# Kernel tuning notes

Hardware: AMD Instinct MI355X
Metric: run time of the kernel (lower is better)

## Reference

```python
import jax, jax.numpy as jnp
import numpy as np

N = 32768      # nodes
E = 524288     # edges (before self-loops)
F_IN = 256     # input feature dim
H = 4          # attention heads
C = 128        # per-head (and output) channels; concat=False -> mean over heads
NEG_SLOPE = 0.2
BN_EPS = 1e-5


def setup_inputs() -> dict:
    key = jax.random.key(0)
    ks = jax.random.split(key, 20)
    s = 0.1
    inp = {
        "x": jax.random.normal(ks[0], (N, F_IN), dtype=jnp.float32),
        "edge_index": jax.random.randint(ks[1], (2, E), 0, N, dtype=jnp.int64),
        # layer 1 (GATConv in=256 -> heads=4, C=128) + BN
        "W1": jax.random.normal(ks[2], (F_IN, H * C), dtype=jnp.float32) * s,
        "as1": jax.random.normal(ks[3], (H, C), dtype=jnp.float32) * s,
        "ad1": jax.random.normal(ks[4], (H, C), dtype=jnp.float32) * s,
        "b1": jnp.zeros((C,), jnp.float32),
        "g1": jnp.ones((C,), jnp.float32),
        "be1": jnp.zeros((C,), jnp.float32),
        # layer 2 (GATConv in=128 -> heads=4, C=128) + BN
        "W2": jax.random.normal(ks[5], (C, H * C), dtype=jnp.float32) * s,
        "as2": jax.random.normal(ks[6], (H, C), dtype=jnp.float32) * s,
        "ad2": jax.random.normal(ks[7], (H, C), dtype=jnp.float32) * s,
        "b2": jnp.zeros((C,), jnp.float32),
        "g2": jnp.ones((C,), jnp.float32),
        "be2": jnp.zeros((C,), jnp.float32),
        # final linear C -> C
        "Wf": jax.random.normal(ks[8], (C, C), dtype=jnp.float32) * s,
        "bf": jnp.zeros((C,), jnp.float32),
    }
    return inp


def _gat_conv(x, src, dst, W, att_src, att_dst, bias):
    # x: [N, Din]; src/dst: [E'] (self-loops already included)
    h = (x @ W).reshape(N, H, C)                     # [N,H,C]
    a_src = jnp.sum(h * att_src, axis=-1)            # [N,H]
    a_dst = jnp.sum(h * att_dst, axis=-1)            # [N,H]
    e = jax.nn.leaky_relu(a_src[src] + a_dst[dst], NEG_SLOPE)  # [E',H]
    # softmax over incoming edges per destination node (segment softmax)
    m = jax.ops.segment_max(e, dst, num_segments=N)  # [N,H]; safe: self-loops
    e = jnp.exp(e - m[dst])
    denom = jax.ops.segment_sum(e, dst, num_segments=N)
    alpha = e / (denom[dst] + 1e-16)                 # [E',H]
    msg = h[src] * alpha[:, :, None]                 # [E',H,C]
    out = jax.ops.segment_sum(msg, dst, num_segments=N)  # [N,H,C]
    return out.mean(axis=1) + bias                   # concat=False -> head mean


def _batch_norm(x, gamma, beta):
    mu = x.mean(axis=0)
    var = x.var(axis=0)  # biased, as torch BN normalization
    return (x - mu) * jax.lax.rsqrt(var + BN_EPS) * gamma + beta


def reference(x, edge_index, W1, as1, ad1, b1, g1, be1,
              W2, as2, ad2, b2, g2, be2, Wf, bf):
    # add self-loops (PyG GATConv default add_self_loops=True)
    loop = jnp.arange(N, dtype=edge_index.dtype)
    src = jnp.concatenate([edge_index[0], loop])
    dst = jnp.concatenate([edge_index[1], loop])

    h = _gat_conv(x, src, dst, W1, as1, ad1, b1)
    h = jax.nn.relu(_batch_norm(h, g1, be1))  # dropout = identity (eval)

    h = _gat_conv(h, src, dst, W2, as2, ad2, b2)
    h = jax.nn.relu(_batch_norm(h, g2, be2))

    return h @ Wf + bf
```

## Files before the change

### kernel.cpp

```cpp
#include <hip/hip_runtime.h>
#include <math.h>

namespace {

constexpr int N    = 32768;
constexpr int E    = 524288;
constexpr int ETOT = E + N;
constexpr int FIN  = 256;
constexpr int H    = 4;
constexpr int C    = 128;
constexpr int HC   = H * C;
constexpr float NEG    = 0.2f;
constexpr float BN_EPS = 1e-5f;

typedef __attribute__((ext_vector_type(8))) short  bf16x8;
typedef __attribute__((ext_vector_type(4))) float  f32x4;

__device__ __forceinline__ float lrelu(float x) { return x >= 0.f ? x : NEG * x; }

__device__ __forceinline__ unsigned short f2b(float f) {
  unsigned u = __float_as_uint(f);
  u = (u + 0x7fffu + ((u >> 16) & 1u)) >> 16;
  return (unsigned short)u;
}
__device__ __forceinline__ unsigned pack2(float a, float b) {
  return (unsigned)f2b(a) | ((unsigned)f2b(b) << 16);
}
__device__ __forceinline__ float blo(unsigned u) { return __uint_as_float(u << 16); }
__device__ __forceinline__ float bhi(unsigned u) { return __uint_as_float(u & 0xffff0000u); }

__device__ __forceinline__ void gll16(const unsigned short* g, unsigned short* l) {
  __builtin_amdgcn_global_load_lds(
      (const __attribute__((address_space(1))) unsigned int*)g,
      (__attribute__((address_space(3))) unsigned int*)l, 16, 0, 0);
}

__global__ void k_cvt4(const float* __restrict__ in, unsigned short* __restrict__ out, int n4) {
  int i = blockIdx.x * blockDim.x + threadIdx.x;
  if (i >= n4) return;
  float4 v = reinterpret_cast<const float4*>(in)[i];
  ushort4 o;
  o.x = f2b(v.x); o.y = f2b(v.y); o.z = f2b(v.z); o.w = f2b(v.w);
  reinterpret_cast<ushort4*>(out)[i] = o;
}

__global__ void k_wcvt(const float* __restrict__ W, unsigned short* __restrict__ Wt,
                       int K, int Nc) {
  int idx = blockIdx.x * blockDim.x + threadIdx.x;
  if (idx >= K * Nc) return;
  int c = idx / K, k = idx - c * K;
  Wt[idx] = f2b(W[(size_t)k * Nc + c]);
}

__global__ void k_wstack(const float* __restrict__ W, unsigned short* __restrict__ Bt,
                         int Din) {
  int idx = blockIdx.x * blockDim.x + threadIdx.x;
  if (idx >= C * 4 * Din) return;
  int c = idx / (4 * Din), r = idx - c * (4 * Din);
  int h = r / Din, k = r - h * Din;
  Bt[idx] = f2b(W[(size_t)k * HC + h * C + c]);
}

__global__ void k_attvec(const float* __restrict__ W, const float* __restrict__ as_,
                         const float* __restrict__ ad_, float* __restrict__ av, int Din) {
  int idx = blockIdx.x * blockDim.x + threadIdx.x;
  if (idx >= 8 * Din) return;
  int j = idx / Din, k = idx - j * Din, h = j & 3;
  const float* a = (j < 4) ? as_ : ad_;
  float s = 0.f;
  for (int c = 0; c < C; ++c) s += W[(size_t)k * HC + h * C + c] * a[h * C + c];
  av[idx] = s;
}

template<int DIN>
__global__ __launch_bounds__(256) void k_attdots(
    const unsigned short* __restrict__ xb, const float* __restrict__ av,
    float* __restrict__ asrc, float* __restrict__ adst)
{
  constexpr int CPL = DIN / 64;
  __shared__ float avs[8 * DIN];
  for (int i = threadIdx.x; i < 8 * DIN; i += 256) avs[i] = av[i];
  __syncthreads();
  int wid = threadIdx.x >> 6, lane = threadIdx.x & 63;
  int n = blockIdx.x * 4 + wid;
  float xv[CPL];
  if constexpr (CPL == 4) {
    uint2 u = *reinterpret_cast<const uint2*>(&xb[(size_t)n * DIN + lane * 4]);
    xv[0] = blo(u.x); xv[1] = bhi(u.x); xv[2] = blo(u.y); xv[3] = bhi(u.y);
  } else {
    unsigned u = *reinterpret_cast<const unsigned*>(&xb[(size_t)n * DIN + lane * 2]);
    xv[0] = blo(u); xv[1] = bhi(u);
  }
  float s[8];
#pragma unroll
  for (int j = 0; j < 8; ++j) {
    float t = 0.f;
#pragma unroll
    for (int q = 0; q < CPL; ++q) t += xv[q] * avs[j * DIN + lane * CPL + q];
    s[j] = t;
  }
#pragma unroll
  for (int off = 1; off < 64; off <<= 1)
#pragma unroll
    for (int j = 0; j < 8; ++j) s[j] += __shfl_xor(s[j], off);
  if (lane == 0) {
    *reinterpret_cast<float4*>(&asrc[n * 4]) = make_float4(s[0], s[1], s[2], s[3]);
    *reinterpret_cast<float4*>(&adst[n * 4]) = make_float4(s[4], s[5], s[6], s[7]);
  }
}

__global__ void k_deg(const int* __restrict__ edst, int* __restrict__ deg) {
  int e = blockIdx.x * blockDim.x + threadIdx.x;
  if (e >= ETOT) return;
  int d = (e < E) ? edst[e] : (e - E);
  atomicAdd(&deg[d], 1);
}

__global__ __launch_bounds__(1024) void k_scan(const int* __restrict__ deg,
                                               int* __restrict__ offs) {
  __shared__ int sums[1024];
  int t = threadIdx.x;
  int base = t * 32;
  int local[32];
  int tot = 0;
#pragma unroll
  for (int i = 0; i < 32; ++i) { local[i] = deg[base + i]; tot += local[i]; }
  sums[t] = tot;
  __syncthreads();
  for (int off = 1; off < 1024; off <<= 1) {
    int v = (t >= off) ? sums[t - off] : 0;
    __syncthreads();
    sums[t] += v;
    __syncthreads();
  }
  int run = (t == 0) ? 0 : sums[t - 1];
#pragma unroll
  for (int i = 0; i < 32; ++i) { offs[base + i] = run; run += local[i]; }
  if (t == 1023) offs[N] = run;
}

__global__ void k_scatter(const int* __restrict__ esrc, const int* __restrict__ edst,
                          const int* __restrict__ offs, int* __restrict__ cursor,
                          int* __restrict__ csrc) {
  int e = blockIdx.x * blockDim.x + threadIdx.x;
  if (e >= ETOT) return;
  int s = (e < E) ? esrc[e] : (e - E);
  int d = (e < E) ? edst[e] : (e - E);
  int pos = offs[d] + atomicAdd(&cursor[d], 1);
  csrc[pos] = s;
}

template<int DIN>
__global__ __launch_bounds__(256) void k_fused_agg(
    const unsigned short* __restrict__ xb, const int* __restrict__ offs,
    const int* __restrict__ csrc, const float* __restrict__ asrc,
    const float* __restrict__ adst, unsigned short* __restrict__ z)
{
  constexpr int CPL = DIN / 64;
  __shared__ float pls[4][64][4];
  __shared__ int   sls[4][64];
  const int wid = threadIdx.x >> 6, lane = threadIdx.x & 63;
  const int n = blockIdx.x * 4 + wid;
  const int beg = offs[n], end = offs[n + 1];
  const float4 bv = *reinterpret_cast<const float4*>(&adst[n * 4]);

  float d0 = 0.f, d1 = 0.f, d2 = 0.f, d3 = 0.f;
  float acc[4][CPL] = {};
  for (int base = beg; base < end; base += 64) {
    int i = base + lane;
    float p0 = 0.f, p1 = 0.f, p2 = 0.f, p3 = 0.f;
    int s = 0;
    if (i < end) {
      s = csrc[i];
      float4 av = *reinterpret_cast<const float4*>(&asrc[s * 4]);
      p0 = __expf(lrelu(av.x + bv.x));
      p1 = __expf(lrelu(av.y + bv.y));
      p2 = __expf(lrelu(av.z + bv.z));
      p3 = __expf(lrelu(av.w + bv.w));
    }
    sls[wid][lane] = s;
    *reinterpret_cast<float4*>(&pls[wid][lane][0]) = make_float4(p0, p1, p2, p3);
    d0 += p0; d1 += p1; d2 += p2; d3 += p3;
    int cnt = end - base; if (cnt > 64) cnt = 64;
#pragma unroll 4
    for (int j = 0; j < cnt; ++j) {
      int sj = sls[wid][j];
      float4 pj = *reinterpret_cast<const float4*>(&pls[wid][j][0]);
      if constexpr (CPL == 4) {
        uint2 u = *reinterpret_cast<const uint2*>(&xb[(size_t)sj * DIN + lane * 4]);
        float c0 = blo(u.x), c1 = bhi(u.x), c2 = blo(u.y), c3 = bhi(u.y);
        acc[0][0] += pj.x * c0; acc[0][1] += pj.x * c1; acc[0][2] += pj.x * c2; acc[0][3] += pj.x * c3;
        acc[1][0] += pj.y * c0; acc[1][1] += pj.y * c1; acc[1][2] += pj.y * c2; acc[1][3] += pj.y * c3;
        acc[2][0] += pj.z * c0; acc[2][1] += pj.z * c1; acc[2][2] += pj.z * c2; acc[2][3] += pj.z * c3;
        acc[3][0] += pj.w * c0; acc[3][1] += pj.w * c1; acc[3][2] += pj.w * c2; acc[3][3] += pj.w * c3;
      } else {
        unsigned u = *reinterpret_cast<const unsigned*>(&xb[(size_t)sj * DIN + lane * 2]);
        float c0 = blo(u), c1 = bhi(u);
        acc[0][0] += pj.x * c0; acc[0][1] += pj.x * c1;
        acc[1][0] += pj.y * c0; acc[1][1] += pj.y * c1;
        acc[2][0] += pj.z * c0; acc[2][1] += pj.z * c1;
        acc[3][0] += pj.w * c0; acc[3][1] += pj.w * c1;
      }
    }
  }
#pragma unroll
  for (int off = 1; off < 64; off <<= 1) {
    d0 += __shfl_xor(d0, off);
    d1 += __shfl_xor(d1, off);
    d2 += __shfl_xor(d2, off);
    d3 += __shfl_xor(d3, off);
  }
  float inv[4];
  inv[0] = 0.25f / (d0 + 1e-16f); inv[1] = 0.25f / (d1 + 1e-16f);
  inv[2] = 0.25f / (d2 + 1e-16f); inv[3] = 0.25f / (d3 + 1e-16f);
  size_t zb = (size_t)n * 4 * DIN;
#pragma unroll
  for (int h = 0; h < 4; ++h) {
    if constexpr (CPL == 4) {
      uint2 o;
      o.x = pack2(acc[h][0] * inv[h], acc[h][1] * inv[h]);
      o.y = pack2(acc[h][2] * inv[h], acc[h][3] * inv[h]);
      *reinterpret_cast<uint2*>(&z[zb + h * DIN + lane * 4]) = o;
    } else {
      *reinterpret_cast<unsigned*>(&z[zb + h * DIN + lane * 2]) =
          pack2(acc[h][0] * inv[h], acc[h][1] * inv[h]);
    }
  }
}

__global__ __launch_bounds__(256) void gemm_bt(
    const unsigned short* __restrict__ A,
    const unsigned short* __restrict__ Bt,
    const float* __restrict__ bias,
    float* __restrict__ O, int K)
{
  __shared__ unsigned short As[64 * 32];
  __shared__ unsigned short Bs[128 * 32];
  const int tid  = threadIdx.x;
  const int wave = tid >> 6, lane = tid & 63;
  const int wr = (wave >> 1) * 32, wc = (wave & 1) * 64;
  const int row0 = blockIdx.x * 64;

  const int fr = lane & 15, kqc = lane >> 4;
  const int sl_r = lane >> 2;
  const int sl_c = lane & 3;

  const int ra  = (wave << 4) + sl_r;
  const int ca  = (sl_c ^ ((ra >> 1) & 3)) * 8;
  const int rb0 = (wave << 5) + sl_r;
  const int cb0 = (sl_c ^ ((rb0 >> 1) & 3)) * 8;
  const int rb1 = rb0 + 16;
  const int cb1 = (sl_c ^ ((rb1 >> 1) & 3)) * 8;

  f32x4 acc[2][4] = {};
  for (int k0 = 0; k0 < K; k0 += 32) {
    gll16(&A [(size_t)(row0 + ra) * K + k0 + ca ], &As[(size_t)(wave << 4) * 32]);
    gll16(&Bt[(size_t)rb0         * K + k0 + cb0], &Bs[(size_t)(wave << 5) * 32]);
    gll16(&Bt[(size_t)rb1         * K + k0 + cb1], &Bs[(size_t)((wave << 5) + 16) * 32]);
    __syncthreads();

    bf16x8 af[2], bfr[4];
#pragma unroll
    for (int m = 0; m < 2; ++m) {
      int r = wr + m * 16 + fr;
      af[m] = *(const bf16x8*)&As[r * 32 + (kqc ^ ((r >> 1) & 3)) * 8];
    }
#pragma unroll
    for (int nn = 0; nn < 4; ++nn) {
      int r = wc + nn * 16 + fr;
      bfr[nn] = *(const bf16x8*)&Bs[r * 32 + (kqc ^ ((r >> 1) & 3)) * 8];
    }
#pragma unroll
    for (int m = 0; m < 2; ++m)
#pragma unroll
      for (int nn = 0; nn < 4; ++nn)
        acc[m][nn] = __builtin_amdgcn_mfma_f32_16x16x32_bf16(af[m], bfr[nn], acc[m][nn], 0, 0, 0);
    __syncthreads();
  }

  const int fq = (lane >> 4) * 4;
#pragma unroll
  for (int m = 0; m < 2; ++m)
#pragma unroll
    for (int nn = 0; nn < 4; ++nn) {
      int col = wc + nn * 16 + fr;
      float bv = bias ? bias[col] : 0.f;
#pragma unroll
      for (int j = 0; j < 4; ++j) {
        int row = row0 + wr + m * 16 + fq + j;
        O[(size_t)row * 128 + col] = acc[m][nn][j] + bv;
      }
    }
}

__global__ __launch_bounds__(128) void k_bn_stats(const float* __restrict__ x,
                                                  float* __restrict__ stats) {
  int c = threadIdx.x;
  int rows = N / gridDim.x;
  int r0 = blockIdx.x * rows;
  float s = 0.f, s2 = 0.f;
  for (int r = r0; r < r0 + rows; ++r) {
    float v = x[(size_t)r * C + c];
    s += v; s2 += v * v;
  }
  atomicAdd(&stats[c], s);
  atomicAdd(&stats[C + c], s2);
}

__global__ void k_bn_apply(const float* __restrict__ stats, const float* __restrict__ g,
                           const float* __restrict__ be, const float* __restrict__ xin,
                           unsigned short* __restrict__ xb) {
  int i = blockIdx.x * blockDim.x + threadIdx.x;
  if (i >= N * C) return;
  int c = i & (C - 1);
  float mu  = stats[c] * (1.f / N);
  float var = stats[C + c] * (1.f / N) - mu * mu;
  float v = (xin[i] - mu) * rsqrtf(var + BN_EPS) * g[c] + be[c];
  xb[i] = f2b(v > 0.f ? v : 0.f);
}

}

extern "C" void kernel_launch(void* const* d_in, const int* in_sizes, int n_in,
                              void* d_out, int out_size, void* d_ws, size_t ws_size,
                              hipStream_t stream) {
  const float* x   = (const float*)d_in[0];
  const int*   ei  = (const int*)d_in[1];
  const float* W1  = (const float*)d_in[2];
  const float* as1 = (const float*)d_in[3];
  const float* ad1 = (const float*)d_in[4];
  const float* g1  = (const float*)d_in[6];
  const float* be1 = (const float*)d_in[7];
  const float* W2  = (const float*)d_in[8];
  const float* as2 = (const float*)d_in[9];
  const float* ad2 = (const float*)d_in[10];
  const float* g2  = (const float*)d_in[12];
  const float* be2 = (const float*)d_in[13];
  const float* Wf  = (const float*)d_in[14];
  const float* bf  = (const float*)d_in[15];
  float* out = (float*)d_out;

  const int* esrc = ei;
  const int* edst = ei + E;

  char* p = (char*)d_ws;
  auto alloc = [&](size_t bytes) {
    char* r = p;
    p += (bytes + 255) & ~size_t(255);
    return r;
  };
  unsigned short* z1   = (unsigned short*)alloc(2ull * N * 4 * FIN);
  unsigned short* xbf  = (unsigned short*)alloc(2ull * N * FIN);
  unsigned short* xmb  = (unsigned short*)alloc(2ull * N * C);
  float*    xm     = (float*)alloc(sizeof(float) * (size_t)N * C);
  unsigned short* Wst1 = (unsigned short*)alloc(2ull * C * 4 * FIN);
  unsigned short* Wst2 = (unsigned short*)alloc(2ull * C * 4 * C);
  unsigned short* Wft  = (unsigned short*)alloc(2ull * C * C);
  float*    av1    = (float*)alloc(sizeof(float) * 8 * FIN);
  float*    av2    = (float*)alloc(sizeof(float) * 8 * C);
  float*    asrc   = (float*)alloc(sizeof(float) * N * 4);
  float*    adst   = (float*)alloc(sizeof(float) * N * 4);
  float*    stats  = (float*)alloc(sizeof(float) * 2 * C);
  int*      deg    = (int*)alloc(sizeof(int) * N);
  int*      offs   = (int*)alloc(sizeof(int) * (N + 16));
  int*      cursor = (int*)alloc(sizeof(int) * N);
  int*      csrc   = (int*)alloc(sizeof(int) * ETOT);
  (void)ws_size; (void)in_sizes; (void)n_in; (void)out_size;

  const int EB = (ETOT + 255) / 256;

  hipMemsetAsync(deg, 0, sizeof(int) * N, stream);
  hipMemsetAsync(cursor, 0, sizeof(int) * N, stream);
  k_deg<<<EB, 256, 0, stream>>>(edst, deg);
  k_scan<<<1, 1024, 0, stream>>>(deg, offs);
  k_scatter<<<EB, 256, 0, stream>>>(esrc, edst, offs, cursor, csrc);

  k_cvt4<<<(N * FIN / 4 + 255) / 256, 256, 0, stream>>>(x, xbf, N * FIN / 4);
  k_wstack<<<(C * 4 * FIN + 255) / 256, 256, 0, stream>>>(W1, Wst1, FIN);
  k_wstack<<<(C * 4 * C + 255) / 256, 256, 0, stream>>>(W2, Wst2, C);
  k_wcvt<<<(C * C + 255) / 256, 256, 0, stream>>>(Wf, Wft, C, C);
  k_attvec<<<(8 * FIN + 255) / 256, 256, 0, stream>>>(W1, as1, ad1, av1, FIN);
  k_attvec<<<(8 * C + 255) / 256, 256, 0, stream>>>(W2, as2, ad2, av2, C);

  k_attdots<FIN><<<N / 4, 256, 0, stream>>>(xbf, av1, asrc, adst);
  k_fused_agg<FIN><<<N / 4, 256, 0, stream>>>(xbf, offs, csrc, asrc, adst, z1);
  gemm_bt<<<N / 64, 256, 0, stream>>>(z1, Wst1, nullptr, xm, 4 * FIN);
  hipMemsetAsync(stats, 0, sizeof(float) * 2 * C, stream);
  k_bn_stats<<<256, C, 0, stream>>>(xm, stats);
  k_bn_apply<<<(N * C) / 256, 256, 0, stream>>>(stats, g1, be1, xm, xmb);

  k_attdots<C><<<N / 4, 256, 0, stream>>>(xmb, av2, asrc, adst);
  k_fused_agg<C><<<N / 4, 256, 0, stream>>>(xmb, offs, csrc, asrc, adst, z1);
  gemm_bt<<<N / 64, 256, 0, stream>>>(z1, Wst2, nullptr, xm, 4 * C);
  hipMemsetAsync(stats, 0, sizeof(float) * 2 * C, stream);
  k_bn_stats<<<256, C, 0, stream>>>(xm, stats);
  k_bn_apply<<<(N * C) / 256, 256, 0, stream>>>(stats, g2, be2, xm, xmb);

  gemm_bt<<<N / 64, 256, 0, stream>>>(xmb, Wft, bf, out, C);
}
```

Baseline: 455.5 us.

## Merge prep kernels, fuse BN-apply into attention dots, split edge softmax into pass

Folds all setup conversions, weight stacking, attention-vector precompute and buffer zeroing into one k_prep launch, replacing several small kernels and memsets. Fuses the layer-1 BN apply and ReLU into the layer-2 attention-dot kernel, which also writes the bf16 activations. Moves the edge exp and denominator work out of the aggregation into a separate k_eexp pass that writes per-edge weights and inverse denominators to a buffer. This cuts launch overhead and shortens the aggregation's critical loop, at the cost of an extra pass that writes and rereads per-edge weights. The aggregation loads csrc and pbuf past the segment end without bounds checks, covered by padded allocations.

```diff
diff --git a/kernel.cpp b/kernel.cpp
--- a/kernel.cpp
+++ b/kernel.cpp
@@ -35,41 +35,89 @@
       (__attribute__((address_space(3))) unsigned int*)l, 16, 0, 0);
 }
 
-__global__ void k_cvt4(const float* __restrict__ in, unsigned short* __restrict__ out, int n4) {
-  int i = blockIdx.x * blockDim.x + threadIdx.x;
-  if (i >= n4) return;
-  float4 v = reinterpret_cast<const float4*>(in)[i];
-  ushort4 o;
-  o.x = f2b(v.x); o.y = f2b(v.y); o.z = f2b(v.z); o.w = f2b(v.w);
-  reinterpret_cast<ushort4*>(out)[i] = o;
-}
-
-__global__ void k_wcvt(const float* __restrict__ W, unsigned short* __restrict__ Wt,
-                       int K, int Nc) {
-  int idx = blockIdx.x * blockDim.x + threadIdx.x;
-  if (idx >= K * Nc) return;
-  int c = idx / K, k = idx - c * K;
-  Wt[idx] = f2b(W[(size_t)k * Nc + c]);
-}
-
-__global__ void k_wstack(const float* __restrict__ W, unsigned short* __restrict__ Bt,
-                         int Din) {
-  int idx = blockIdx.x * blockDim.x + threadIdx.x;
-  if (idx >= C * 4 * Din) return;
-  int c = idx / (4 * Din), r = idx - c * (4 * Din);
-  int h = r / Din, k = r - h * Din;
-  Bt[idx] = f2b(W[(size_t)k * HC + h * C + c]);
-}
-
-__global__ void k_attvec(const float* __restrict__ W, const float* __restrict__ as_,
-                         const float* __restrict__ ad_, float* __restrict__ av, int Din) {
-  int idx = blockIdx.x * blockDim.x + threadIdx.x;
-  if (idx >= 8 * Din) return;
-  int j = idx / Din, k = idx - j * Din, h = j & 3;
-  const float* a = (j < 4) ? as_ : ad_;
-  float s = 0.f;
-  for (int c = 0; c < C; ++c) s += W[(size_t)k * HC + h * C + c] * a[h * C + c];
-  av[idx] = s;
+constexpr int PB_X   = (N * FIN / 4) / 256;
+constexpr int PB_W1  = (C * 4 * FIN) / 256;
+constexpr int PB_W2  = (C * 4 * C) / 256;
+constexpr int PB_WF  = (C * C) / 256;
+constexpr int PB_AV1 = (8 * FIN) / 256;
+constexpr int PB_AV2 = (8 * C) / 256;
+constexpr int PB_Z   = (2 * N + 512) / 256;
+constexpr int PB_TOT = PB_X + PB_W1 + PB_W2 + PB_WF + PB_AV1 + PB_AV2 + PB_Z;
+
+__global__ __launch_bounds__(256) void k_prep(
+    const float* __restrict__ x,
+    const float* __restrict__ W1, const float* __restrict__ W2, const float* __restrict__ Wf,
+    const float* __restrict__ as1, const float* __restrict__ ad1,
+    const float* __restrict__ as2, const float* __restrict__ ad2,
+    unsigned short* __restrict__ xbf, unsigned short* __restrict__ Wst1,
+    unsigned short* __restrict__ Wst2, unsigned short* __restrict__ Wft,
+    float* __restrict__ av1, float* __restrict__ av2,
+    int* __restrict__ deg, int* __restrict__ cursor,
+    float* __restrict__ stats1, float* __restrict__ stats2)
+{
+  int b = blockIdx.x, t = threadIdx.x;
+  if (b < PB_X) {
+    int i = b * 256 + t;
+    float4 v = reinterpret_cast<const float4*>(x)[i];
+    ushort4 o;
+    o.x = f2b(v.x); o.y = f2b(v.y); o.z = f2b(v.z); o.w = f2b(v.w);
+    reinterpret_cast<ushort4*>(xbf)[i] = o;
+    return;
+  }
+  b -= PB_X;
+  if (b < PB_W1) {
+    int idx = b * 256 + t;
+    int c = idx / (4 * FIN), r = idx - c * (4 * FIN);
+    int h = r / FIN, k = r - h * FIN;
+    Wst1[idx] = f2b(W1[(size_t)k * HC + h * C + c]);
+    return;
+  }
+  b -= PB_W1;
+  if (b < PB_W2) {
+    int idx = b * 256 + t;
+    int c = idx / (4 * C), r = idx - c * (4 * C);
+    int h = r / C, k = r - h * C;
+    Wst2[idx] = f2b(W2[(size_t)k * HC + h * C + c]);
+    return;
+  }
+  b -= PB_W2;
+  if (b < PB_WF) {
+    int idx = b * 256 + t;
+    int c = idx / C, k = idx - c * C;
+    Wft[idx] = f2b(Wf[(size_t)k * C + c]);
+    return;
+  }
+  b -= PB_WF;
+  if (b < PB_AV1) {
+    int idx = b * 256 + t;
+    int j = idx / FIN, k = idx - j * FIN, h = j & 3;
+    const float* a = (j < 4) ? as1 : ad1;
+    float s = 0.f;
+    for (int c = 0; c < C; ++c) s += W1[(size_t)k * HC + h * C + c] * a[h * C + c];
+    av1[idx] = s;
+    return;
+  }
+  b -= PB_AV1;
+  if (b < PB_AV2) {
+    int idx = b * 256 + t;
+    int j = idx / C, k = idx - j * C, h = j & 3;
+    const float* a = (j < 4) ? as2 : ad2;
+    float s = 0.f;
+    for (int c = 0; c < C; ++c) s += W2[(size_t)k * HC + h * C + c] * a[h * C + c];
+    av2[idx] = s;
+    return;
+  }
+  b -= PB_AV2;
+  {
+    int i = b * 256 + t;
+    if (i < N) deg[i] = 0;
+    else if (i < 2 * N) cursor[i - N] = 0;
+    else {
+      int i2 = i - 2 * N;
+      if (i2 < 256) stats1[i2] = 0.f;
+      else if (i2 < 512) stats2[i2 - 256] = 0.f;
+    }
+  }
 }
 
 template<int DIN>
@@ -109,6 +157,45 @@
   }
 }
 
+__global__ __launch_bounds__(256) void k_attdots_bn(
+    const float* __restrict__ xm, const float* __restrict__ stats,
+    const float* __restrict__ g, const float* __restrict__ be,
+    const float* __restrict__ av, unsigned short* __restrict__ xmb,
+    float* __restrict__ asrc, float* __restrict__ adst)
+{
+  __shared__ float avs[8 * C];
+  __shared__ float bnsc[C], bnsh[C];
+  int t = threadIdx.x;
+  for (int i = t; i < 8 * C; i += 256) avs[i] = av[i];
+  if (t < C) {
+    float mu  = stats[t] * (1.f / N);
+    float var = stats[C + t] * (1.f / N) - mu * mu;
+    float sc  = rsqrtf(var + BN_EPS) * g[t];
+    bnsc[t] = sc;
+    bnsh[t] = be[t] - mu * sc;
+  }
+  __syncthreads();
+  int wid = t >> 6, lane = t & 63;
+  int n = blockIdx.x * 4 + wid;
+  int c = lane * 2;
+  float2 xv = *reinterpret_cast<const float2*>(&xm[(size_t)n * C + c]);
+  float v0 = fmaxf(xv.x * bnsc[c]     + bnsh[c],     0.f);
+  float v1 = fmaxf(xv.y * bnsc[c + 1] + bnsh[c + 1], 0.f);
+  *reinterpret_cast<unsigned*>(&xmb[(size_t)n * C + c]) = pack2(v0, v1);
+  float s[8];
+#pragma unroll
+  for (int j = 0; j < 8; ++j)
+    s[j] = v0 * avs[j * C + c] + v1 * avs[j * C + c + 1];
+#pragma unroll
+  for (int off = 1; off < 64; off <<= 1)
+#pragma unroll
+    for (int j = 0; j < 8; ++j) s[j] += __shfl_xor(s[j], off);
+  if (lane == 0) {
+    *reinterpret_cast<float4*>(&asrc[n * 4]) = make_float4(s[0], s[1], s[2], s[3]);
+    *reinterpret_cast<float4*>(&adst[n * 4]) = make_float4(s[4], s[5], s[6], s[7]);
+  }
+}
+
 __global__ void k_deg(const int* __restrict__ edst, int* __restrict__ deg) {
   int e = blockIdx.x * blockDim.x + threadIdx.x;
   if (e >= ETOT) return;
@@ -150,11 +237,44 @@
   csrc[pos] = s;
 }
 
+__global__ __launch_bounds__(256) void k_eexp(
+    const int* __restrict__ offs, const int* __restrict__ csrc,
+    const float* __restrict__ asrc, const float* __restrict__ adst,
+    float* __restrict__ pbuf, float* __restrict__ denominv)
+{
+  int gid = blockIdx.x * 256 + threadIdx.x;
+  int n = gid >> 4, l = gid & 15;
+  int beg = offs[n], end = offs[n + 1];
+  const float4 bv = *reinterpret_cast<const float4*>(&adst[n * 4]);
+  float d0 = 0.f, d1 = 0.f, d2 = 0.f, d3 = 0.f;
+  for (int i = beg + l; i < end; i += 16) {
+    int s = csrc[i];
+    float4 av = *reinterpret_cast<const float4*>(&asrc[s * 4]);
+    float p0 = __expf(lrelu(av.x + bv.x));
+    float p1 = __expf(lrelu(av.y + bv.y));
+    float p2 = __expf(lrelu(av.z + bv.z));
+    float p3 = __expf(lrelu(av.w + bv.w));
+    *reinterpret_cast<float4*>(&pbuf[(size_t)i * 4]) = make_float4(p0, p1, p2, p3);
+    d0 += p0; d1 += p1; d2 += p2; d3 += p3;
+  }
+#pragma unroll
+  for (int off = 1; off < 16; off <<= 1) {
+    d0 += __shfl_xor(d0, off);
+    d1 += __shfl_xor(d1, off);
+    d2 += __shfl_xor(d2, off);
+    d3 += __shfl_xor(d3, off);
+  }
+  if (l == 0)
+    *reinterpret_cast<float4*>(&denominv[n * 4]) =
+        make_float4(0.25f / (d0 + 1e-16f), 0.25f / (d1 + 1e-16f),
+                    0.25f / (d2 + 1e-16f), 0.25f / (d3 + 1e-16f));
+}
+
 template<int DIN>
 __global__ __launch_bounds__(256) void k_fused_agg(
     const unsigned short* __restrict__ xb, const int* __restrict__ offs,
-    const int* __restrict__ csrc, const float* __restrict__ asrc,
-    const float* __restrict__ adst, unsigned short* __restrict__ z)
+    const int* __restrict__ csrc, const float* __restrict__ pbuf,
+    const float* __restrict__ denominv, unsigned short* __restrict__ z)
 {
   constexpr int CPL = DIN / 64;
   __shared__ float pls[4][64][4];
@@ -162,25 +282,14 @@
   const int wid = threadIdx.x >> 6, lane = threadIdx.x & 63;
   const int n = blockIdx.x * 4 + wid;
   const int beg = offs[n], end = offs[n + 1];
-  const float4 bv = *reinterpret_cast<const float4*>(&adst[n * 4]);
-
-  float d0 = 0.f, d1 = 0.f, d2 = 0.f, d3 = 0.f;
+
   float acc[4][CPL] = {};
   for (int base = beg; base < end; base += 64) {
     int i = base + lane;
-    float p0 = 0.f, p1 = 0.f, p2 = 0.f, p3 = 0.f;
-    int s = 0;
-    if (i < end) {
-      s = csrc[i];
-      float4 av = *reinterpret_cast<const float4*>(&asrc[s * 4]);
-      p0 = __expf(lrelu(av.x + bv.x));
-      p1 = __expf(lrelu(av.y + bv.y));
-      p2 = __expf(lrelu(av.z + bv.z));
-      p3 = __expf(lrelu(av.w + bv.w));
-    }
+    int s = csrc[i];
+    float4 pv = *reinterpret_cast<const float4*>(&pbuf[(size_t)i * 4]);
     sls[wid][lane] = s;
-    *reinterpret_cast<float4*>(&pls[wid][lane][0]) = make_float4(p0, p1, p2, p3);
-    d0 += p0; d1 += p1; d2 += p2; d3 += p3;
+    *reinterpret_cast<float4*>(&pls[wid][lane][0]) = pv;
     int cnt = end - base; if (cnt > 64) cnt = 64;
 #pragma unroll 4
     for (int j = 0; j < cnt; ++j) {
@@ -203,16 +312,8 @@
       }
     }
   }
-#pragma unroll
-  for (int off = 1; off < 64; off <<= 1) {
-    d0 += __shfl_xor(d0, off);
-    d1 += __shfl_xor(d1, off);
-    d2 += __shfl_xor(d2, off);
-    d3 += __shfl_xor(d3, off);
-  }
-  float inv[4];
-  inv[0] = 0.25f / (d0 + 1e-16f); inv[1] = 0.25f / (d1 + 1e-16f);
-  inv[2] = 0.25f / (d2 + 1e-16f); inv[3] = 0.25f / (d3 + 1e-16f);
+  const float4 iv4 = *reinterpret_cast<const float4*>(&denominv[n * 4]);
+  const float inv[4] = { iv4.x, iv4.y, iv4.z, iv4.w };
   size_t zb = (size_t)n * 4 * DIN;
 #pragma unroll
   for (int h = 0; h < 4; ++h) {
@@ -353,6 +454,7 @@
   unsigned short* xbf  = (unsigned short*)alloc(2ull * N * FIN);
   unsigned short* xmb  = (unsigned short*)alloc(2ull * N * C);
   float*    xm     = (float*)alloc(sizeof(float) * (size_t)N * C);
+  float*    pbuf   = (float*)alloc(sizeof(float) * (size_t)(ETOT + 64) * 4);
   unsigned short* Wst1 = (unsigned short*)alloc(2ull * C * 4 * FIN);
   unsigned short* Wst2 = (unsigned short*)alloc(2ull * C * 4 * C);
   unsigned short* Wft  = (unsigned short*)alloc(2ull * C * C);
@@ -360,41 +462,37 @@
   float*    av2    = (float*)alloc(sizeof(float) * 8 * C);
   float*    asrc   = (float*)alloc(sizeof(float) * N * 4);
   float*    adst   = (float*)alloc(sizeof(float) * N * 4);
-  float*    stats  = (float*)alloc(sizeof(float) * 2 * C);
+  float*    denominv = (float*)alloc(sizeof(float) * N * 4);
+  float*    stats1 = (float*)alloc(sizeof(float) * 2 * C);
+  float*    stats2 = (float*)alloc(sizeof(float) * 2 * C);
   int*      deg    = (int*)alloc(sizeof(int) * N);
   int*      offs   = (int*)alloc(sizeof(int) * (N + 16));
   int*      cursor = (int*)alloc(sizeof(int) * N);
-  int*      csrc   = (int*)alloc(sizeof(int) * ETOT);
+  int*      csrc   = (int*)alloc(sizeof(int) * (ETOT + 64));
   (void)ws_size; (void)in_sizes; (void)n_in; (void)out_size;
 
   const int EB = (ETOT + 255) / 256;
 
-  hipMemsetAsync(deg, 0, sizeof(int) * N, stream);
-  hipMemsetAsync(cursor, 0, sizeof(int) * N, stream);
+  k_prep<<<PB_TOT, 256, 0, stream>>>(x, W1, W2, Wf, as1, ad1, as2, ad2,
+                                     xbf, Wst1, Wst2, Wft, av1, av2,
+                                     deg, cursor, stats1, stats2);
+
   k_deg<<<EB, 256, 0, stream>>>(edst, deg);
   k_scan<<<1, 1024, 0, stream>>>(deg, offs);
   k_scatter<<<EB, 256, 0, stream>>>(esrc, edst, offs, cursor, csrc);
 
-  k_cvt4<<<(N * FIN / 4 + 255) / 256, 256, 0, stream>>>(x, xbf, N * FIN / 4);
-  k_wstack<<<(C * 4 * FIN + 255) / 256, 256, 0, stream>>>(W1, Wst1, FIN);
-  k_wstack<<<(C * 4 * C + 255) / 256, 256, 0, stream>>>(W2, Wst2, C);
-  k_wcvt<<<(C * C + 255) / 256, 256, 0, stream>>>(Wf, Wft, C, C);
-  k_attvec<<<(8 * FIN + 255) / 256, 256, 0, stream>>>(W1, as1, ad1, av1, FIN);
-  k_attvec<<<(8 * C + 255) / 256, 256, 0, stream>>>(W2, as2, ad2, av2, C);
-
   k_attdots<FIN><<<N / 4, 256, 0, stream>>>(xbf, av1, asrc, adst);
-  k_fused_agg<FIN><<<N / 4, 256, 0, stream>>>(xbf, offs, csrc, asrc, adst, z1);
+  k_eexp<<<(N * 16) / 256, 256, 0, stream>>>(offs, csrc, asrc, adst, pbuf, denominv);
+  k_fused_agg<FIN><<<N / 4, 256, 0, stream>>>(xbf, offs, csrc, pbuf, denominv, z1);
   gemm_bt<<<N / 64, 256, 0, stream>>>(z1, Wst1, nullptr, xm, 4 * FIN);
-  hipMemsetAsync(stats, 0, sizeof(float) * 2 * C, stream);
-  k_bn_stats<<<256, C, 0, stream>>>(xm, stats);
-  k_bn_apply<<<(N * C) / 256, 256, 0, stream>>>(stats, g1, be1, xm, xmb);
-
-  k_attdots<C><<<N / 4, 256, 0, stream>>>(xmb, av2, asrc, adst);
-  k_fused_agg<C><<<N / 4, 256, 0, stream>>>(xmb, offs, csrc, asrc, adst, z1);
+  k_bn_stats<<<256, C, 0, stream>>>(xm, stats1);
+
+  k_attdots_bn<<<N / 4, 256, 0, stream>>>(xm, stats1, g1, be1, av2, xmb, asrc, adst);
+  k_eexp<<<(N * 16) / 256, 256, 0, stream>>>(offs, csrc, asrc, adst, pbuf, denominv);
+  k_fused_agg<C><<<N / 4, 256, 0, stream>>>(xmb, offs, csrc, pbuf, denominv, z1);
   gemm_bt<<<N / 64, 256, 0, stream>>>(z1, Wst2, nullptr, xm, 4 * C);
-  hipMemsetAsync(stats, 0, sizeof(float) * 2 * C, stream);
-  k_bn_stats<<<256, C, 0, stream>>>(xm, stats);
-  k_bn_apply<<<(N * C) / 256, 256, 0, stream>>>(stats, g2, be2, xm, xmb);
+  k_bn_stats<<<256, C, 0, stream>>>(xm, stats2);
+  k_bn_apply<<<(N * C) / 256, 256, 0, stream>>>(stats2, g2, be2, xm, xmb);
 
   gemm_bt<<<N / 64, 256, 0, stream>>>(xmb, Wft, bf, out, C);
 }
```

Result: faster. 432.8 us (-5.0%).
